# Kernel optimization log

Hardware: AMD Instinct MI355X
Metric: run time of the kernel (lower is better)

## Reference

```python
import jax, jax.numpy as jnp
import numpy as np

N, H, V = 8192, 1024, 32000
IGNORE_INDEX = -100
LABEL_SMOOTHING = 0.0
LOGIT_SCALE = 1.0


def setup_inputs() -> dict:
    key = jax.random.key(0)
    k1, k2, k3 = jax.random.split(key, 3)
    x = jax.random.normal(k1, (N, H), dtype=jnp.float32)
    weight = jax.random.normal(k2, (V, H), dtype=jnp.float32) * 0.02
    bias = jnp.zeros((V,), dtype=jnp.float32)
    target = jax.random.randint(k3, (N,), 0, V, dtype=jnp.int64)
    return {"x": x, "weight": weight, "bias": bias, "target": target}


def reference(x, weight, bias, target):
    # logits: [N, V]; fused kernel never materializes this fully, but math is identical
    logits = (x @ weight.T + bias) * LOGIT_SCALE
    lse = jax.nn.logsumexp(logits.astype(jnp.float32), axis=-1)  # [N]
    valid = target != IGNORE_INDEX
    safe_t = jnp.where(valid, target, 0)
    tgt_logit = jnp.take_along_axis(logits, safe_t[:, None], axis=-1)[:, 0]
    loss_i = lse - tgt_logit
    if LABEL_SMOOTHING > 0:
        eps = LABEL_SMOOTHING / V
        z = (-eps * logits).sum(-1)
        loss_i = loss_i * (1.0 - LABEL_SMOOTHING) + (z + LABEL_SMOOTHING * lse)
    loss_i = jnp.where(valid, loss_i, 0.0)
    total = jnp.maximum(valid.sum(), 1)
    # reduction == 'mean': each per-token loss divided by total, then summed
    return loss_i.sum() / total
```

## Files before the change

kernel.cpp:

```cpp
#include <hip/hip_runtime.h>
#include <math.h>

typedef int    intx8    __attribute__((ext_vector_type(8)));
typedef float  floatx16 __attribute__((ext_vector_type(16)));

#define N_ROWS 8192
#define H_DIM  1024
#define V_DIM  32000
#define IGNORE_INDEX (-100)

#define S_SPLITS 25
#define TILES_PER_SPLIT 10
#define BM 128
#define BN 128
#define BK 64

#define LOG2E 1.4426950408889634f
#define LN2   0.6931471805599453f

__global__ __launch_bounds__(256) void convert_fp8(const float* __restrict__ in,
                                                   unsigned char* __restrict__ out,
                                                   int R, float scale) {
  const int r = blockIdx.x * 256 + threadIdx.x;
  const int u = blockIdx.y;
  const float4* src = (const float4*)(in + (size_t)r * H_DIM + u * 16);
  uint4 res;
#pragma unroll
  for (int j = 0; j < 4; ++j) {
    const float4 v = src[j];
    int p = __builtin_amdgcn_cvt_pk_fp8_f32(v.x * scale, v.y * scale, 0, false);
    p = __builtin_amdgcn_cvt_pk_fp8_f32(v.z * scale, v.w * scale, p, true);
    ((int*)&res)[j] = p;
  }
  *(uint4*)(out + ((size_t)u * R + r) * 16) = res;
}

__global__ __launch_bounds__(256, 3) void flce_main(const unsigned char* __restrict__ xs,
                                                    const unsigned char* __restrict__ wsb,
                                                    const float* __restrict__ bias,
                                                    float* __restrict__ partials) {
  __shared__ __align__(16) unsigned char smA[4 * 128 * 16];
  __shared__ __align__(16) unsigned char smB[4 * 128 * 16];

  const int tid  = threadIdx.x;
  const int lane = tid & 63;
  const int w    = tid >> 6;
  const int l31  = lane & 31;
  const int half = lane >> 5;
  const int wm   = w >> 1;
  const int wn   = w & 1;
  const int row0 = blockIdx.x * BM;
  const int sidx = blockIdx.y;

  const int rbA = (wm * 64 + l31) * 16;
  const int rbB = (wn * 64 + l31) * 16;
  const int uo  = half * 4096;

  float l_state[32];
#pragma unroll
  for (int i = 0; i < 32; ++i) l_state[i] = 0.f;

#pragma unroll 1
  for (int ct = 0; ct < TILES_PER_SPLIT; ++ct) {
    const int n0 = (sidx * TILES_PER_SPLIT + ct) * BN;
    floatx16 acc[2][2];
#pragma unroll
    for (int mb = 0; mb < 2; ++mb)
#pragma unroll
      for (int nb = 0; nb < 2; ++nb)
#pragma unroll
        for (int i = 0; i < 16; ++i) acc[mb][nb][i] = 0.f;

#pragma unroll 1
    for (int k0i = 0; k0i < H_DIM / BK; ++k0i) {
      const int ub = k0i * 4;
      __syncthreads();
#pragma unroll
      for (int j = 0; j < 2; ++j) {
        const int s = j * 4 + w;
        const int u = s >> 1;
        const int rh = s & 1;
        __builtin_amdgcn_global_load_lds(
            (const __attribute__((address_space(1))) void*)(xs + ((size_t)(ub + u) * N_ROWS + row0 + rh * 64 + lane) * 16),
            (__attribute__((address_space(3))) void*)(smA + s * 1024 + lane * 16),
            16, 0, 0);
        __builtin_amdgcn_global_load_lds(
            (const __attribute__((address_space(1))) void*)(wsb + ((size_t)(ub + u) * V_DIM + n0 + rh * 64 + lane) * 16),
            (__attribute__((address_space(3))) void*)(smB + s * 1024 + lane * 16),
            16, 0, 0);
      }
      __syncthreads();

      union { intx8 v; uint4 q[2]; } a[2], b[2];
#pragma unroll
      for (int mb = 0; mb < 2; ++mb) {
        a[mb].q[0] = *(const uint4*)(smA + uo + mb * 512 + rbA);
        a[mb].q[1] = *(const uint4*)(smA + uo + 2048 + mb * 512 + rbA);
      }
#pragma unroll
      for (int nb = 0; nb < 2; ++nb) {
        b[nb].q[0] = *(const uint4*)(smB + uo + nb * 512 + rbB);
        b[nb].q[1] = *(const uint4*)(smB + uo + 2048 + nb * 512 + rbB);
      }
#pragma unroll
      for (int mb = 0; mb < 2; ++mb)
#pragma unroll
        for (int nb = 0; nb < 2; ++nb)
          acc[mb][nb] = __builtin_amdgcn_mfma_scale_f32_32x32x64_f8f6f4(
              a[mb].v, b[nb].v, acc[mb][nb],
              0, 0,
              0, 0x7F7F7F7F,
              0, 0x7F7F7F7F);
    }

    const float b0 = bias[n0 + wn * 64 + l31] * LOG2E;
    const float b1 = bias[n0 + wn * 64 + 32 + l31] * LOG2E;
#pragma unroll
    for (int mb = 0; mb < 2; ++mb)
#pragma unroll
      for (int r = 0; r < 16; ++r)
        l_state[mb * 16 + r] += exp2f(acc[mb][0][r] + b0) + exp2f(acc[mb][1][r] + b1);
  }

#pragma unroll
  for (int s = 0; s < 32; ++s) {
    float v = l_state[s];
#pragma unroll
    for (int off = 1; off < 32; off <<= 1) v += __shfl_xor(v, off, 64);
    l_state[s] = v;
  }

  __syncthreads();
  float* comb = (float*)smA;
  if (wn == 0 && l31 == 0) {
#pragma unroll
    for (int s = 0; s < 32; ++s) {
      const int mb = s >> 4, r = s & 15;
      const int row = wm * 64 + mb * 32 + 4 * half + (r & 3) + 8 * (r >> 2);
      comb[row] = l_state[s];
    }
  }
  __syncthreads();
  if (wn == 1 && l31 == 0) {
#pragma unroll
    for (int s = 0; s < 32; ++s) {
      const int mb = s >> 4, r = s & 15;
      const int row = wm * 64 + mb * 32 + 4 * half + (r & 3) + 8 * (r >> 2);
      partials[(size_t)(row0 + row) * S_SPLITS + sidx] = comb[row] + l_state[s];
    }
  }
}

__global__ __launch_bounds__(256) void tgt_kernel(const float* __restrict__ x,
                                                  const float* __restrict__ wgt,
                                                  const float* __restrict__ bias,
                                                  const int* __restrict__ target,
                                                  float* __restrict__ tgt_logit) {
  const int r = blockIdx.x * 4 + (threadIdx.x >> 6);
  const int lane = threadIdx.x & 63;
  const int t = target[r];
  const int tt = (t == IGNORE_INDEX) ? 0 : t;
  const float4* xr = (const float4*)(x + (size_t)r * H_DIM);
  const float4* wr = (const float4*)(wgt + (size_t)tt * H_DIM);
  float acc = 0.f;
#pragma unroll
  for (int i = 0; i < 4; ++i) {
    const float4 a = xr[lane + i * 64];
    const float4 b = wr[lane + i * 64];
    acc += a.x * b.x + a.y * b.y + a.z * b.z + a.w * b.w;
  }
#pragma unroll
  for (int off = 32; off >= 1; off >>= 1) acc += __shfl_xor(acc, off, 64);
  if (lane == 0) tgt_logit[r] = acc + bias[tt];
}

__global__ __launch_bounds__(256) void loss_rows(const float* __restrict__ partials,
                                                 const float* __restrict__ tgt_logit,
                                                 const int* __restrict__ target,
                                                 float* __restrict__ bsums) {
  const int r = blockIdx.x * 256 + threadIdx.x;
  float l = 0.f;
#pragma unroll
  for (int s = 0; s < S_SPLITS; ++s) l += partials[(size_t)r * S_SPLITS + s];
  const float lse = LN2 * __log2f(l);
  const bool valid = (target[r] != IGNORE_INDEX);
  float loss = valid ? (lse - tgt_logit[r]) : 0.f;
  float cnt  = valid ? 1.f : 0.f;
  const int lane = threadIdx.x & 63;
  const int w = threadIdx.x >> 6;
#pragma unroll
  for (int off = 32; off >= 1; off >>= 1) {
    loss += __shfl_xor(loss, off, 64);
    cnt  += __shfl_xor(cnt, off, 64);
  }
  __shared__ float sl[4], sc[4];
  if (lane == 0) { sl[w] = loss; sc[w] = cnt; }
  __syncthreads();
  if (threadIdx.x == 0) {
    float S = 0.f, C = 0.f;
    for (int i = 0; i < 4; ++i) { S += sl[i]; C += sc[i]; }
    bsums[blockIdx.x] = S;
    bsums[32 + blockIdx.x] = C;
  }
}

__global__ void finalize(const float* __restrict__ bsums, float* __restrict__ out) {
  const int t = threadIdx.x;
  float s = (t < 32) ? bsums[t] : 0.f;
  float c = (t < 32) ? bsums[32 + t] : 0.f;
#pragma unroll
  for (int off = 32; off >= 1; off >>= 1) {
    s += __shfl_xor(s, off, 64);
    c += __shfl_xor(c, off, 64);
  }
  if (t == 0) out[0] = s / fmaxf(c, 1.f);
}

extern "C" void kernel_launch(void* const* d_in, const int* in_sizes, int n_in,
                              void* d_out, int out_size, void* d_ws, size_t ws_size,
                              hipStream_t stream) {
  const float* x    = (const float*)d_in[0];
  const float* wgt  = (const float*)d_in[1];
  const float* bias = (const float*)d_in[2];
  const int*   tgt  = (const int*)d_in[3];
  float* out = (float*)d_out;

  char* ws = (char*)d_ws;
  const size_t XS8 = (size_t)N_ROWS * H_DIM;
  const size_t WS8 = (size_t)V_DIM * H_DIM;
  const size_t PB  = (size_t)N_ROWS * S_SPLITS * 4;
  unsigned char* xs8 = (unsigned char*)ws;
  unsigned char* ws8 = (unsigned char*)(ws + XS8);
  float* partials = (float*)(ws + XS8 + WS8);
  float* tgt_lg   = (float*)(ws + XS8 + WS8 + PB);
  float* bsums    = (float*)(ws + XS8 + WS8 + PB + (size_t)N_ROWS * 4);

  convert_fp8<<<dim3(N_ROWS / 256, H_DIM / 16), 256, 0, stream>>>(x, xs8, N_ROWS, LOG2E);
  convert_fp8<<<dim3(V_DIM / 256, H_DIM / 16), 256, 0, stream>>>(wgt, ws8, V_DIM, 1.0f);
  tgt_kernel<<<N_ROWS / 4, 256, 0, stream>>>(x, wgt, bias, tgt, tgt_lg);
  flce_main<<<dim3(N_ROWS / BM, S_SPLITS), 256, 0, stream>>>(xs8, ws8, bias, partials);
  loss_rows<<<N_ROWS / 256, 256, 0, stream>>>(partials, tgt_lg, tgt, bsums);
  finalize<<<1, 64, 0, stream>>>(bsums, out);
}
```

Baseline: 586.9 us.

## Enlarge GEMM tiles to 256x128x128 and pad vocab with masked bias

Each block now covers 256 rows with a 128-wide K step, and every wave computes a 64x128 output slab, so register and LDS reuse rises and fewer barriers are needed per FLOP. The vocabulary is padded to 32768 with a precomputed log2e-scaled bias where padded columns get -1e30, giving evenly divisible splits. The cross-wave LDS combine is dropped because each wave owns full tile columns. The costs are lower occupancy (2 blocks per CU), a few percent of wasted padded compute, and reliance on uninitialized padded weight bytes not decoding to NaN.

```diff
diff --git a/kernel.cpp b/kernel.cpp
--- a/kernel.cpp
+++ b/kernel.cpp
@@ -7,20 +7,21 @@
 #define N_ROWS 8192
 #define H_DIM  1024
 #define V_DIM  32000
+#define V_PAD  32768
 #define IGNORE_INDEX (-100)
 
-#define S_SPLITS 25
-#define TILES_PER_SPLIT 10
-#define BM 128
+#define S_SPLITS 16
+#define TILES_PER_SPLIT 16
+#define BM 256
 #define BN 128
-#define BK 64
+#define BK 128
 
 #define LOG2E 1.4426950408889634f
 #define LN2   0.6931471805599453f
 
 __global__ __launch_bounds__(256) void convert_fp8(const float* __restrict__ in,
                                                    unsigned char* __restrict__ out,
-                                                   int R, float scale) {
+                                                   int Rstride, float scale) {
   const int r = blockIdx.x * 256 + threadIdx.x;
   const int u = blockIdx.y;
   const float4* src = (const float4*)(in + (size_t)r * H_DIM + u * 16);
@@ -32,29 +33,30 @@
     p = __builtin_amdgcn_cvt_pk_fp8_f32(v.z * scale, v.w * scale, p, true);
     ((int*)&res)[j] = p;
   }
-  *(uint4*)(out + ((size_t)u * R + r) * 16) = res;
-}
-
-__global__ __launch_bounds__(256, 3) void flce_main(const unsigned char* __restrict__ xs,
+  *(uint4*)(out + ((size_t)u * Rstride + r) * 16) = res;
+}
+
+__global__ __launch_bounds__(256) void pad_bias(const float* __restrict__ bias,
+                                                float* __restrict__ biasp) {
+  const int i = blockIdx.x * 256 + threadIdx.x;
+  biasp[i] = (i < V_DIM) ? bias[i] * LOG2E : -1e30f;
+}
+
+__global__ __launch_bounds__(256, 2) void flce_main(const unsigned char* __restrict__ xs,
                                                     const unsigned char* __restrict__ wsb,
-                                                    const float* __restrict__ bias,
+                                                    const float* __restrict__ biasp,
                                                     float* __restrict__ partials) {
-  __shared__ __align__(16) unsigned char smA[4 * 128 * 16];
-  __shared__ __align__(16) unsigned char smB[4 * 128 * 16];
+  __shared__ __align__(16) unsigned char smA[8 * 256 * 16];
+  __shared__ __align__(16) unsigned char smB[8 * 128 * 16];
 
   const int tid  = threadIdx.x;
   const int lane = tid & 63;
   const int w    = tid >> 6;
   const int l31  = lane & 31;
   const int half = lane >> 5;
-  const int wm   = w >> 1;
-  const int wn   = w & 1;
+  const int wr   = w * 64;
   const int row0 = blockIdx.x * BM;
   const int sidx = blockIdx.y;
-
-  const int rbA = (wm * 64 + l31) * 16;
-  const int rbB = (wn * 64 + l31) * 16;
-  const int uo  = half * 4096;
 
   float l_state[32];
 #pragma unroll
@@ -63,63 +65,77 @@
 #pragma unroll 1
   for (int ct = 0; ct < TILES_PER_SPLIT; ++ct) {
     const int n0 = (sidx * TILES_PER_SPLIT + ct) * BN;
-    floatx16 acc[2][2];
+    floatx16 acc[2][4];
 #pragma unroll
     for (int mb = 0; mb < 2; ++mb)
 #pragma unroll
-      for (int nb = 0; nb < 2; ++nb)
+      for (int nb = 0; nb < 4; ++nb)
 #pragma unroll
         for (int i = 0; i < 16; ++i) acc[mb][nb][i] = 0.f;
 
 #pragma unroll 1
     for (int k0i = 0; k0i < H_DIM / BK; ++k0i) {
-      const int ub = k0i * 4;
+      const int ub = k0i * 8;
       __syncthreads();
 #pragma unroll
-      for (int j = 0; j < 2; ++j) {
-        const int s = j * 4 + w;
-        const int u = s >> 1;
-        const int rh = s & 1;
+      for (int j = 0; j < 8; ++j) {
+        const int c = j * 4 + w;
+        const int u = c >> 2;
+        const int rb = c & 3;
         __builtin_amdgcn_global_load_lds(
-            (const __attribute__((address_space(1))) void*)(xs + ((size_t)(ub + u) * N_ROWS + row0 + rh * 64 + lane) * 16),
-            (__attribute__((address_space(3))) void*)(smA + s * 1024 + lane * 16),
+            (const __attribute__((address_space(1))) void*)(xs + ((size_t)(ub + u) * N_ROWS + row0 + rb * 64 + lane) * 16),
+            (__attribute__((address_space(3))) void*)(smA + ((u * 256 + rb * 64 + lane) * 16)),
             16, 0, 0);
+      }
+#pragma unroll
+      for (int j = 0; j < 4; ++j) {
+        const int c = j * 4 + w;
+        const int u = c >> 1;
+        const int rb = c & 1;
         __builtin_amdgcn_global_load_lds(
-            (const __attribute__((address_space(1))) void*)(wsb + ((size_t)(ub + u) * V_DIM + n0 + rh * 64 + lane) * 16),
-            (__attribute__((address_space(3))) void*)(smB + s * 1024 + lane * 16),
+            (const __attribute__((address_space(1))) void*)(wsb + ((size_t)(ub + u) * V_PAD + n0 + rb * 64 + lane) * 16),
+            (__attribute__((address_space(3))) void*)(smB + ((u * 128 + rb * 64 + lane) * 16)),
             16, 0, 0);
       }
       __syncthreads();
 
-      union { intx8 v; uint4 q[2]; } a[2], b[2];
-#pragma unroll
-      for (int mb = 0; mb < 2; ++mb) {
-        a[mb].q[0] = *(const uint4*)(smA + uo + mb * 512 + rbA);
-        a[mb].q[1] = *(const uint4*)(smA + uo + 2048 + mb * 512 + rbA);
-      }
-#pragma unroll
-      for (int nb = 0; nb < 2; ++nb) {
-        b[nb].q[0] = *(const uint4*)(smB + uo + nb * 512 + rbB);
-        b[nb].q[1] = *(const uint4*)(smB + uo + 2048 + nb * 512 + rbB);
-      }
-#pragma unroll
-      for (int mb = 0; mb < 2; ++mb)
-#pragma unroll
-        for (int nb = 0; nb < 2; ++nb)
-          acc[mb][nb] = __builtin_amdgcn_mfma_scale_f32_32x32x64_f8f6f4(
-              a[mb].v, b[nb].v, acc[mb][nb],
-              0, 0,
-              0, 0x7F7F7F7F,
-              0, 0x7F7F7F7F);
+#pragma unroll
+      for (int s2 = 0; s2 < 2; ++s2) {
+        const int ua = s2 * 4 + half * 2;
+        union { intx8 v; uint4 q[2]; } a[2], b[4];
+#pragma unroll
+        for (int mb = 0; mb < 2; ++mb) {
+          a[mb].q[0] = *(const uint4*)(smA + ((ua * 256 + wr + mb * 32 + l31) * 16));
+          a[mb].q[1] = *(const uint4*)(smA + (((ua + 1) * 256 + wr + mb * 32 + l31) * 16));
+        }
+#pragma unroll
+        for (int nb = 0; nb < 4; ++nb) {
+          b[nb].q[0] = *(const uint4*)(smB + ((ua * 128 + nb * 32 + l31) * 16));
+          b[nb].q[1] = *(const uint4*)(smB + (((ua + 1) * 128 + nb * 32 + l31) * 16));
+        }
+#pragma unroll
+        for (int mb = 0; mb < 2; ++mb)
+#pragma unroll
+          for (int nb = 0; nb < 4; ++nb)
+            acc[mb][nb] = __builtin_amdgcn_mfma_scale_f32_32x32x64_f8f6f4(
+                a[mb].v, b[nb].v, acc[mb][nb],
+                0, 0,
+                0, 0x7F7F7F7F,
+                0, 0x7F7F7F7F);
+      }
     }
 
-    const float b0 = bias[n0 + wn * 64 + l31] * LOG2E;
-    const float b1 = bias[n0 + wn * 64 + 32 + l31] * LOG2E;
+    float bnb[4];
+#pragma unroll
+    for (int nb = 0; nb < 4; ++nb) bnb[nb] = biasp[n0 + nb * 32 + l31];
 #pragma unroll
     for (int mb = 0; mb < 2; ++mb)
 #pragma unroll
-      for (int r = 0; r < 16; ++r)
-        l_state[mb * 16 + r] += exp2f(acc[mb][0][r] + b0) + exp2f(acc[mb][1][r] + b1);
+      for (int r = 0; r < 16; ++r) {
+        float s = exp2f(acc[mb][0][r] + bnb[0]) + exp2f(acc[mb][1][r] + bnb[1])
+                + exp2f(acc[mb][2][r] + bnb[2]) + exp2f(acc[mb][3][r] + bnb[3]);
+        l_state[mb * 16 + r] += s;
+      }
   }
 
 #pragma unroll
@@ -130,23 +146,12 @@
     l_state[s] = v;
   }
 
-  __syncthreads();
-  float* comb = (float*)smA;
-  if (wn == 0 && l31 == 0) {
+  if (l31 == 0) {
 #pragma unroll
     for (int s = 0; s < 32; ++s) {
       const int mb = s >> 4, r = s & 15;
-      const int row = wm * 64 + mb * 32 + 4 * half + (r & 3) + 8 * (r >> 2);
-      comb[row] = l_state[s];
-    }
-  }
-  __syncthreads();
-  if (wn == 1 && l31 == 0) {
-#pragma unroll
-    for (int s = 0; s < 32; ++s) {
-      const int mb = s >> 4, r = s & 15;
-      const int row = wm * 64 + mb * 32 + 4 * half + (r & 3) + 8 * (r >> 2);
-      partials[(size_t)(row0 + row) * S_SPLITS + sidx] = comb[row] + l_state[s];
+      const int row = wr + mb * 32 + 4 * half + (r & 3) + 8 * (r >> 2);
+      partials[(size_t)(row0 + row) * S_SPLITS + sidx] = l_state[s];
     }
   }
 }
@@ -227,18 +232,21 @@
 
   char* ws = (char*)d_ws;
   const size_t XS8 = (size_t)N_ROWS * H_DIM;
-  const size_t WS8 = (size_t)V_DIM * H_DIM;
+  const size_t WS8 = (size_t)V_PAD * H_DIM;
+  const size_t BP  = (size_t)V_PAD * 4;
   const size_t PB  = (size_t)N_ROWS * S_SPLITS * 4;
   unsigned char* xs8 = (unsigned char*)ws;
   unsigned char* ws8 = (unsigned char*)(ws + XS8);
-  float* partials = (float*)(ws + XS8 + WS8);
-  float* tgt_lg   = (float*)(ws + XS8 + WS8 + PB);
-  float* bsums    = (float*)(ws + XS8 + WS8 + PB + (size_t)N_ROWS * 4);
+  float* biasp    = (float*)(ws + XS8 + WS8);
+  float* partials = (float*)(ws + XS8 + WS8 + BP);
+  float* tgt_lg   = (float*)(ws + XS8 + WS8 + BP + PB);
+  float* bsums    = (float*)(ws + XS8 + WS8 + BP + PB + (size_t)N_ROWS * 4);
 
   convert_fp8<<<dim3(N_ROWS / 256, H_DIM / 16), 256, 0, stream>>>(x, xs8, N_ROWS, LOG2E);
-  convert_fp8<<<dim3(V_DIM / 256, H_DIM / 16), 256, 0, stream>>>(wgt, ws8, V_DIM, 1.0f);
+  convert_fp8<<<dim3(V_DIM / 256, H_DIM / 16), 256, 0, stream>>>(wgt, ws8, V_PAD, 1.0f);
+  pad_bias<<<V_PAD / 256, 256, 0, stream>>>(bias, biasp);
   tgt_kernel<<<N_ROWS / 4, 256, 0, stream>>>(x, wgt, bias, tgt, tgt_lg);
-  flce_main<<<dim3(N_ROWS / BM, S_SPLITS), 256, 0, stream>>>(xs8, ws8, bias, partials);
+  flce_main<<<dim3(N_ROWS / BM, S_SPLITS), 256, 0, stream>>>(xs8, ws8, biasp, partials);
   loss_rows<<<N_ROWS / 256, 256, 0, stream>>>(partials, tgt_lg, tgt, bsums);
   finalize<<<1, 64, 0, stream>>>(bsums, out);
 }
```

Measured after the change: 495.9 us. -15.5%, faster.
